# Performance work log

Measured on AMD Instinct MI355X. Metric: run time of the kernel, lower is better.

Reference implementation:

```python
import jax, jax.numpy as jnp
import numpy as np

K = 9          # knn_num
EPS = 1e-5     # BatchNorm eps


def _conv2d(x, w, stride):
    # x: NCHW, w: OIHW, VALID padding
    return jax.lax.conv_general_dilated(
        x, w, window_strides=stride, padding='VALID',
        dimension_numbers=('NCHW', 'OIHW', 'NCHW'))


def _bn_relu(x, gamma, beta):
    # training-mode BatchNorm2d (biased batch stats over N,H,W) + ReLU
    mean = jnp.mean(x, axis=(0, 2, 3), keepdims=True)
    var = jnp.var(x, axis=(0, 2, 3), keepdims=True)
    xhat = (x - mean) * jax.lax.rsqrt(var + EPS)
    return jax.nn.relu(xhat * gamma[None, :, None, None] + beta[None, :, None, None])


def setup_inputs() -> dict:
    key = jax.random.key(0)
    ks = jax.random.split(key, 5)
    B, C, N = 16, 128, 2048
    features = jax.random.normal(ks[0], (B, C, N, 1), dtype=jnp.float32)
    fan1 = 2 * C * 1 * 3
    W1 = jax.random.normal(ks[1], (C, 2 * C, 1, 3), dtype=jnp.float32) / np.sqrt(fan1)
    b1 = jnp.zeros((C,), dtype=jnp.float32)
    g1 = jnp.ones((C,), dtype=jnp.float32)
    beta1 = jnp.zeros((C,), dtype=jnp.float32)
    fan2 = C * 1 * 3
    W2 = jax.random.normal(ks[2], (C, C, 1, 3), dtype=jnp.float32) / np.sqrt(fan2)
    b2 = jnp.zeros((C,), dtype=jnp.float32)
    g2 = jnp.ones((C,), dtype=jnp.float32)
    beta2 = jnp.zeros((C,), dtype=jnp.float32)
    return {"features": features, "W1": W1, "b1": b1, "g1": g1, "beta1": beta1,
            "W2": W2, "b2": b2, "g2": g2, "beta2": beta2}


def reference(features, W1, b1, g1, beta1, W2, b2, g2, beta2):
    B, C, N, _ = features.shape
    x = features.reshape(B, C, N)
    # pairwise_distance[b,i,j] = -||x_i||^2 + 2 x_i.x_j - ||x_j||^2 = -||x_i - x_j||^2
    xx = jnp.sum(x * x, axis=1)                      # (B, N)
    inner = jnp.einsum('bci,bcj->bij', x, x)          # (B, N, N)
    pd = 2.0 * inner - xx[:, :, None] - xx[:, None, :]
    _, idx = jax.lax.top_k(pd, K)                     # (B, N, K) nearest neighbors (incl. self)
    xT = jnp.transpose(x, (0, 2, 1))                  # (B, N, C)
    feature = xT[jnp.arange(B)[:, None, None], idx]   # (B, N, K, C) gathered neighbors
    xc = xT[:, :, None, :]                            # (B, N, 1, C)
    diff = xc - feature
    # torch: cat(x, (x - f) - |x - f|) along channel dim -> (B, N, K, 2C)
    edge = jnp.concatenate(
        [jnp.broadcast_to(xc, diff.shape), diff - jnp.abs(diff)], axis=3)
    edge = jnp.transpose(edge, (0, 3, 1, 2))          # (B, 2C, N, K)
    h = _conv2d(edge, W1, (1, 3)) + b1[None, :, None, None]   # (B, C, N, 3)
    h = _bn_relu(h, g1, beta1)
    h = _conv2d(h, W2, (1, 1)) + b2[None, :, None, None]       # (B, C, N, 1)
    h = _bn_relu(h, g2, beta2)
    return h
```

## Files before the change

### kernel.cpp

```cpp
#include <hip/hip_runtime.h>
#include <cstddef>

#define BATCH 16
#define CH    128
#define NPTS  2048
#define KNN   9

typedef const __attribute__((address_space(1))) void* gptr_t;
typedef __attribute__((address_space(3))) void* lptr_t;

__global__ void k_transpose(const float* __restrict__ x, float* __restrict__ xT) {
  __shared__ float tile[32][33];
  int b = blockIdx.z;
  int n0 = blockIdx.x * 32, c0 = blockIdx.y * 32;
  int tx = threadIdx.x, ty = threadIdx.y;
#pragma unroll
  for (int i = 0; i < 4; ++i) {
    int cc = c0 + ty + i * 8;
    tile[ty + i * 8][tx] = x[((size_t)b * CH + cc) * NPTS + n0 + tx];
  }
  __syncthreads();
#pragma unroll
  for (int i = 0; i < 4; ++i) {
    int nn = n0 + ty + i * 8;
    xT[((size_t)b * NPTS + nn) * CH + c0 + tx] = tile[tx][ty + i * 8];
  }
}

__global__ void k_xx_pw(const float* __restrict__ x, float* __restrict__ xx) {
  int g = blockIdx.x * 256 + threadIdx.x;
  int b = g >> 11, n = g & (NPTS - 1);
  const float* p = x + (size_t)b * CH * NPTS + n;
  float s[128];
#pragma unroll
  for (int c = 0; c < 128; ++c) {
    float v = p[(size_t)c * NPTS];
    s[c] = __fmul_rn(v, v);
  }
  float lane[16];
#pragma unroll
  for (int l = 0; l < 16; ++l) {
    lane[l] = __fadd_rn(
        __fadd_rn(__fadd_rn(s[l], s[16 + l]), __fadd_rn(s[32 + l], s[48 + l])),
        __fadd_rn(__fadd_rn(s[64 + l], s[80 + l]), __fadd_rn(s[96 + l], s[112 + l])));
  }
  float m8[8];
#pragma unroll
  for (int i = 0; i < 8; ++i) m8[i] = __fadd_rn(lane[i], lane[i + 8]);
  float n4[4];
#pragma unroll
  for (int i = 0; i < 4; ++i) n4[i] = __fadd_rn(m8[i], m8[i + 4]);
  float p2[2];
#pragma unroll
  for (int i = 0; i < 2; ++i) p2[i] = __fadd_rn(n4[i], n4[i + 2]);
  xx[g] = __fadd_rn(p2[0], p2[1]);
}

__global__ __launch_bounds__(256) void k_knn_np(const float* __restrict__ x,
                                                const float* __restrict__ xx,
                                                int* __restrict__ idxout) {
  __shared__ __align__(16) char smraw[65536];
  float (*rowT)[64] = (float (*)[64])smraw;
  float (*colT)[64] = (float (*)[64])(smraw + 32768);
  float (*mv)[145] = (float (*)[145])smraw;
  unsigned short (*mi)[145] = (unsigned short (*)[145])(smraw + 37120);

  int b = blockIdx.y;
  int n0 = blockIdx.x * 64;
  int tid = threadIdx.x;
  int tx = tid & 15, ty = tid >> 4;

  const float* gb = x + (size_t)b * CH * NPTS;

#pragma unroll
  for (int i = 0; i < 8; ++i) {
    int e = i * 1024 + tid * 4;
    const float* ga = gb + (size_t)(e >> 6) * NPTS + n0 + (e & 63);
    __builtin_amdgcn_global_load_lds((gptr_t)ga, (lptr_t)(&rowT[0][0] + e), 16, 0, 0);
  }

  float tv[4][9];
  int   ti[4][9];
#pragma unroll
  for (int m = 0; m < 4; ++m)
#pragma unroll
    for (int s = 0; s < 9; ++s) { tv[m][s] = -3.4e38f; ti[m][s] = 0x7fffffff; }

  float xr[4];
#pragma unroll
  for (int m = 0; m < 4; ++m) xr[m] = xx[(size_t)b * NPTS + n0 + ty * 4 + m];

  for (int jt = 0; jt < NPTS; jt += 64) {
    __syncthreads();
#pragma unroll
    for (int i = 0; i < 8; ++i) {
      int e = i * 1024 + tid * 4;
      const float* ga = gb + (size_t)(e >> 6) * NPTS + jt + (e & 63);
      __builtin_amdgcn_global_load_lds((gptr_t)ga, (lptr_t)(&colT[0][0] + e), 16, 0, 0);
    }
    asm volatile("s_waitcnt vmcnt(0)" ::: "memory");
    __syncthreads();

    float acc[4][4];
#pragma unroll
    for (int m = 0; m < 4; ++m)
#pragma unroll
      for (int nn = 0; nn < 4; ++nn) acc[m][nn] = 0.f;

#pragma unroll 4
    for (int k = 0; k < CH; ++k) {
      float a[4], bv[4];
      *(float4*)a  = *(const float4*)&rowT[k][ty * 4];
      *(float4*)bv = *(const float4*)&colT[k][tx * 4];
#pragma unroll
      for (int m = 0; m < 4; ++m)
#pragma unroll
        for (int nn = 0; nn < 4; ++nn)
          acc[m][nn] = __builtin_fmaf(a[m], bv[nn], acc[m][nn]);
    }

#pragma unroll
    for (int nn = 0; nn < 4; ++nn) {
      int j = jt + tx * 4 + nn;
      float xc = xx[(size_t)b * NPTS + j];
#pragma unroll
      for (int m = 0; m < 4; ++m) {
        float val = __fsub_rn(__fsub_rn(__fmul_rn(2.0f, acc[m][nn]), xr[m]), xc);
        if (val > tv[m][8]) {
          float cv = val; int ci = j;
#pragma unroll
          for (int s = 0; s < 9; ++s) {
            bool sw = cv > tv[m][s];
            float t1 = tv[m][s]; int t2 = ti[m][s];
            tv[m][s] = sw ? cv : t1;  ti[m][s] = sw ? ci : t2;
            cv = sw ? t1 : cv;        ci = sw ? t2 : ci;
          }
        }
      }
    }
  }

  __syncthreads();
#pragma unroll
  for (int m = 0; m < 4; ++m) {
    int row = ty * 4 + m;
#pragma unroll
    for (int s = 0; s < 9; ++s) {
      mv[row][tx * 9 + s] = tv[m][s];
      mi[row][tx * 9 + s] = (unsigned short)ti[m][s];
    }
  }
  __syncthreads();
  if (tid < 64) {
    int row = tid;
    size_t base = ((size_t)b * NPTS + n0 + row) * KNN;
    for (int s = 0; s < KNN; ++s) {
      float best = -3.4e38f; int bj = 0x7fffffff; int bq = 0;
      for (int q = 0; q < 144; ++q) {
        float v = mv[row][q]; int jj = (int)mi[row][q];
        if (v > best || (v == best && jj < bj)) { best = v; bj = jj; bq = q; }
      }
      mv[row][bq] = -3.4e38f;
      idxout[base + s] = bj;
    }
  }
}

__global__ void k_prep(const float* __restrict__ W1, const float* __restrict__ W2,
                       float* __restrict__ At, float* __restrict__ W2t) {
  int g = blockIdx.x * 256 + threadIdx.x;
  if (g < 512 * 128) {
    int k = g / 128, o = g % 128;
    float v;
    if (k < 384) v = W1[(size_t)o * 768 + 384 + k];
    else {
      int c = k - 384;
      v = W1[(size_t)o * 768 + c * 3] + W1[(size_t)o * 768 + c * 3 + 1] +
          W1[(size_t)o * 768 + c * 3 + 2];
    }
    At[(size_t)k * 128 + o] = v;
  }
  if (g < 384 * 128) {
    int k = g / 128, o = g % 128;
    W2t[(size_t)k * 128 + o] = W2[(size_t)o * 384 + k];
  }
}

#define NN1 8
__global__ __launch_bounds__(256) void k_conv1(const float* __restrict__ xT,
                                               const int* __restrict__ knn_idx,
                                               const float* __restrict__ At,
                                               const float* __restrict__ bias1,
                                               float* __restrict__ h1) {
  __shared__ float dminL[NN1][KNN][132];
  __shared__ float xnL[NN1][132];
  __shared__ float AL[32][128];
  __shared__ int   idxL[NN1][KNN];
  int b = blockIdx.y;
  int n0 = blockIdx.x * NN1;
  int tid = threadIdx.x;

  if (tid < NN1 * KNN) {
    int n = tid / KNN, k = tid % KNN;
    idxL[n][k] = knn_idx[((size_t)b * NPTS + n0 + n) * KNN + k];
  }
  {
    int n = tid >> 5, q = tid & 31;
    float4 v = *(const float4*)&xT[((size_t)b * NPTS + n0 + n) * CH + q * 4];
    *(float4*)&xnL[n][q * 4] = v;
  }
  __syncthreads();
#pragma unroll
  for (int i = 0; i < 9; ++i) {
    int e = tid + i * 256;
    int rrow = e >> 5, q = e & 31;
    int n = rrow / KNN, k = rrow % KNN;
    int j = idxL[n][k];
    float4 xj = *(const float4*)&xT[((size_t)b * NPTS + j) * CH + q * 4];
    float4 xn = *(const float4*)&xnL[n][q * 4];
    float4 d;
    d.x = 2.0f * fminf(xn.x - xj.x, 0.0f);
    d.y = 2.0f * fminf(xn.y - xj.y, 0.0f);
    d.z = 2.0f * fminf(xn.z - xj.z, 0.0f);
    d.w = 2.0f * fminf(xn.w - xj.w, 0.0f);
    *(float4*)&dminL[n][k][q * 4] = d;
  }

  int n = tid & (NN1 - 1);
  int og = tid >> 3;
  float acc[4][3];
#pragma unroll
  for (int o = 0; o < 4; ++o)
#pragma unroll
    for (int t = 0; t < 3; ++t) acc[o][t] = 0.f;

  for (int kc = 0; kc < 16; ++kc) {
    __syncthreads();
#pragma unroll
    for (int i = 0; i < 4; ++i) {
      int e = tid + i * 256;
      int kk = e >> 5, q = e & 31;
      *(float4*)&AL[kk][q * 4] = *(const float4*)&At[(size_t)(kc * 32 + kk) * 128 + q * 4];
    }
    __syncthreads();
    if (kc < 12) {
#pragma unroll 4
      for (int kk = 0; kk < 32; ++kk) {
        int k = kc * 32 + kk;
        int c = k / 3, r = k - c * 3;
        float a[4];
        *(float4*)a = *(const float4*)&AL[kk][og * 4];
        float b0 = dminL[n][r][c];
        float b1 = dminL[n][3 + r][c];
        float b2 = dminL[n][6 + r][c];
#pragma unroll
        for (int o = 0; o < 4; ++o) {
          acc[o][0] = fmaf(a[o], b0, acc[o][0]);
          acc[o][1] = fmaf(a[o], b1, acc[o][1]);
          acc[o][2] = fmaf(a[o], b2, acc[o][2]);
        }
      }
    } else {
#pragma unroll 4
      for (int kk = 0; kk < 32; ++kk) {
        int c = (kc - 12) * 32 + kk;
        float a[4];
        *(float4*)a = *(const float4*)&AL[kk][og * 4];
        float b0 = xnL[n][c];
#pragma unroll
        for (int o = 0; o < 4; ++o) {
          acc[o][0] = fmaf(a[o], b0, acc[o][0]);
          acc[o][1] = fmaf(a[o], b0, acc[o][1]);
          acc[o][2] = fmaf(a[o], b0, acc[o][2]);
        }
      }
    }
  }
#pragma unroll
  for (int o = 0; o < 4; ++o) {
    int oo = og * 4 + o;
    float bs = bias1[oo];
    size_t base = ((size_t)(b * CH + oo) * NPTS + n0 + n) * 3;
#pragma unroll
    for (int t = 0; t < 3; ++t) h1[base + t] = acc[o][t] + bs;
  }
}

__global__ void k_stats_partial(const float* __restrict__ src, double* __restrict__ psum,
                                double* __restrict__ psq, int slablen) {
  __shared__ double ls[256], lq[256];
  int blk = blockIdx.x;
  const float* p = src + (size_t)blk * slablen;
  double s = 0.0, q = 0.0;
  for (int i = threadIdx.x; i < slablen; i += 256) {
    double v = (double)p[i];
    s += v; q = fma(v, v, q);
  }
  ls[threadIdx.x] = s; lq[threadIdx.x] = q;
  __syncthreads();
  for (int off = 128; off > 0; off >>= 1) {
    if (threadIdx.x < off) {
      ls[threadIdx.x] += ls[threadIdx.x + off];
      lq[threadIdx.x] += lq[threadIdx.x + off];
    }
    __syncthreads();
  }
  if (threadIdx.x == 0) { psum[blk] = ls[0]; psq[blk] = lq[0]; }
}

__global__ void k_stats_final(const double* __restrict__ psum, const double* __restrict__ psq,
                              const float* __restrict__ gamma, const float* __restrict__ beta,
                              float* __restrict__ aout, float* __restrict__ cout_,
                              double inv_n) {
  int c = threadIdx.x;
  if (c < CH) {
    double s = 0.0, q = 0.0;
    for (int b = 0; b < BATCH; ++b) { s += psum[b * CH + c]; q += psq[b * CH + c]; }
    double mean = s * inv_n;
    double var = q * inv_n - mean * mean;
    double a = (double)gamma[c] / sqrt(var + 1e-5);
    aout[c] = (float)a;
    cout_[c] = (float)((double)beta[c] - mean * a);
  }
}

__global__ __launch_bounds__(256) void k_conv2(const float* __restrict__ h1,
                                               const float* __restrict__ W2t,
                                               const float* __restrict__ bias2,
                                               const float* __restrict__ a1,
                                               const float* __restrict__ c1,
                                               float* __restrict__ out) {
  __shared__ float actL[384][36];
  __shared__ float WL[16][128];
  int b = blockIdx.y, n0 = blockIdx.x * 32, tid = threadIdx.x;
#pragma unroll
  for (int i = 0; i < 12; ++i) {
    int e = tid + i * 256;
    int c = e / 24, q = e % 24;
    float4 v = *(const float4*)&h1[((size_t)(b * CH + c) * NPTS + n0) * 3 + q * 4];
    float aa = a1[c], cc = c1[c];
    float vv[4] = {v.x, v.y, v.z, v.w};
#pragma unroll
    for (int s = 0; s < 4; ++s) {
      int f = q * 4 + s;
      int nn = f / 3, t = f - nn * 3;
      actL[c * 3 + t][nn] = fmaxf(0.0f, fmaf(vv[s], aa, cc));
    }
  }
  int ng = tid & 7, og = tid >> 3;
  float acc[4][4];
#pragma unroll
  for (int o = 0; o < 4; ++o)
#pragma unroll
    for (int nn = 0; nn < 4; ++nn) acc[o][nn] = 0.f;

  for (int kc = 0; kc < 24; ++kc) {
    __syncthreads();
#pragma unroll
    for (int i = 0; i < 2; ++i) {
      int e = tid + i * 256;
      int kk = e >> 5, q = e & 31;
      *(float4*)&WL[kk][q * 4] = *(const float4*)&W2t[(size_t)(kc * 16 + kk) * 128 + q * 4];
    }
    __syncthreads();
#pragma unroll 4
    for (int kk = 0; kk < 16; ++kk) {
      float a[4], bv[4];
      *(float4*)a  = *(const float4*)&WL[kk][og * 4];
      *(float4*)bv = *(const float4*)&actL[kc * 16 + kk][ng * 4];
#pragma unroll
      for (int o = 0; o < 4; ++o)
#pragma unroll
        for (int nn = 0; nn < 4; ++nn) acc[o][nn] = fmaf(a[o], bv[nn], acc[o][nn]);
    }
  }
#pragma unroll
  for (int o = 0; o < 4; ++o) {
    int oo = og * 4 + o;
    float bs = bias2[oo];
    size_t base = (size_t)(b * CH + oo) * NPTS + n0 + ng * 4;
#pragma unroll
    for (int nn = 0; nn < 4; ++nn) out[base + nn] = acc[o][nn] + bs;
  }
}

__global__ void k_bnrelu(float* __restrict__ out, const float* __restrict__ a2,
                         const float* __restrict__ c2) {
  int g = blockIdx.x * 256 + threadIdx.x;
  int c = (g >> 11) & 127;
  float v = out[g];
  out[g] = fmaxf(0.0f, fmaf(v, a2[c], c2[c]));
}

extern "C" void kernel_launch(void* const* d_in, const int* in_sizes, int n_in,
                              void* d_out, int out_size, void* d_ws, size_t ws_size,
                              hipStream_t stream) {
  const float* x   = (const float*)d_in[0];
  const float* W1  = (const float*)d_in[1];
  const float* b1  = (const float*)d_in[2];
  const float* g1  = (const float*)d_in[3];
  const float* be1 = (const float*)d_in[4];
  const float* W2  = (const float*)d_in[5];
  const float* b2  = (const float*)d_in[6];
  const float* g2  = (const float*)d_in[7];
  const float* be2 = (const float*)d_in[8];
  float* out = (float*)d_out;

  char* ws = (char*)d_ws;
  float*  xT      = (float*) (ws);
  float*  xx      = (float*) (ws + 16777216);
  int*    knn_idx = (int*)   (ws + 16908288);
  float*  At      = (float*) (ws + 18087936);
  float*  W2t     = (float*) (ws + 18350080);
  float*  h1      = (float*) (ws + 18546688);
  double* psum    = (double*)(ws + 68878336);
  double* psq     = (double*)(ws + 68894720);
  float*  a1      = (float*) (ws + 68911104);
  float*  c1      = (float*) (ws + 68911616);
  float*  a2      = (float*) (ws + 68912128);
  float*  c2      = (float*) (ws + 68912640);

  k_transpose<<<dim3(NPTS / 32, CH / 32, BATCH), dim3(32, 8), 0, stream>>>(x, xT);
  k_xx_pw<<<(BATCH * NPTS) / 256, 256, 0, stream>>>(x, xx);
  k_knn_np<<<dim3(NPTS / 64, BATCH), 256, 0, stream>>>(x, xx, knn_idx);
  k_prep<<<256, 256, 0, stream>>>(W1, W2, At, W2t);
  k_conv1<<<dim3(NPTS / NN1, BATCH), 256, 0, stream>>>(xT, knn_idx, At, b1, h1);
  k_stats_partial<<<BATCH * CH, 256, 0, stream>>>(h1, psum, psq, NPTS * 3);
  k_stats_final<<<1, 128, 0, stream>>>(psum, psq, g1, be1, a1, c1,
                                       1.0 / (double)(BATCH * NPTS * 3));
  k_conv2<<<dim3(NPTS / 32, BATCH), 256, 0, stream>>>(h1, W2t, b2, a1, c1, out);
  k_stats_partial<<<BATCH * CH, 256, 0, stream>>>(out, psum, psq, NPTS);
  k_stats_final<<<1, 128, 0, stream>>>(psum, psq, g2, be2, a2, c2,
                                       1.0 / (double)(BATCH * NPTS));
  k_bnrelu<<<(BATCH * CH * NPTS) / 256, 256, 0, stream>>>(out, a2, c2);
}
```

Measured before the change: 864.9 us.

## Enlarge kNN distance tile to 128x128 with 8x8 register blocking per thread

The kNN kernel's block tile grows from 64x64 to 128x128 points, and each thread now computes an 8x8 block of the inner-product matrix instead of 4x4. Dynamic LDS is raised to 128KB to hold the larger row and column panels. This raises arithmetic intensity per LDS read and halves the number of column-tile passes per block. In exchange it uses many more registers (a top-9 list for 8 rows plus 64 accumulators), and with one block per CU at 256 threads the grid drops to 256 blocks, so occupancy and latency hiding fall.

```diff
diff --git a/kernel.cpp b/kernel.cpp
--- a/kernel.cpp
+++ b/kernel.cpp
@@ -5,6 +5,8 @@
 #define CH    128
 #define NPTS  2048
 #define KNN   9
+#define BM    128
+#define BN    128
 
 typedef const __attribute__((address_space(1))) void* gptr_t;
 typedef __attribute__((address_space(3))) void* lptr_t;
@@ -56,102 +58,107 @@
   xx[g] = __fadd_rn(p2[0], p2[1]);
 }
 
-__global__ __launch_bounds__(256) void k_knn_np(const float* __restrict__ x,
-                                                const float* __restrict__ xx,
-                                                int* __restrict__ idxout) {
-  __shared__ __align__(16) char smraw[65536];
-  float (*rowT)[64] = (float (*)[64])smraw;
-  float (*colT)[64] = (float (*)[64])(smraw + 32768);
-  float (*mv)[145] = (float (*)[145])smraw;
-  unsigned short (*mi)[145] = (unsigned short (*)[145])(smraw + 37120);
+__global__ __launch_bounds__(256, 1) void k_knn_np(const float* __restrict__ x,
+                                                   const float* __restrict__ xx,
+                                                   int* __restrict__ idxout) {
+  extern __shared__ __align__(16) char smraw[];
+  float (*rowT)[BM] = (float (*)[BM])smraw;
+  float (*colT)[BN] = (float (*)[BN])(smraw + 65536);
+  float (*mv)[144] = (float (*)[144])smraw;
+  unsigned short (*mi)[144] = (unsigned short (*)[144])(smraw + 73728);
 
   int b = blockIdx.y;
-  int n0 = blockIdx.x * 64;
+  int n0 = blockIdx.x * BM;
   int tid = threadIdx.x;
   int tx = tid & 15, ty = tid >> 4;
 
   const float* gb = x + (size_t)b * CH * NPTS;
 
 #pragma unroll
-  for (int i = 0; i < 8; ++i) {
+  for (int i = 0; i < 16; ++i) {
     int e = i * 1024 + tid * 4;
-    const float* ga = gb + (size_t)(e >> 6) * NPTS + n0 + (e & 63);
+    const float* ga = gb + (size_t)(e >> 7) * NPTS + n0 + (e & 127);
     __builtin_amdgcn_global_load_lds((gptr_t)ga, (lptr_t)(&rowT[0][0] + e), 16, 0, 0);
   }
 
-  float tv[4][9];
-  int   ti[4][9];
-#pragma unroll
-  for (int m = 0; m < 4; ++m)
-#pragma unroll
-    for (int s = 0; s < 9; ++s) { tv[m][s] = -3.4e38f; ti[m][s] = 0x7fffffff; }
-
-  float xr[4];
-#pragma unroll
-  for (int m = 0; m < 4; ++m) xr[m] = xx[(size_t)b * NPTS + n0 + ty * 4 + m];
-
-  for (int jt = 0; jt < NPTS; jt += 64) {
-    __syncthreads();
-#pragma unroll
-    for (int i = 0; i < 8; ++i) {
+  float tv[8][9];
+  int   ti[8][9];
+#pragma unroll
+  for (int r = 0; r < 8; ++r)
+#pragma unroll
+    for (int s = 0; s < 9; ++s) { tv[r][s] = -3.4e38f; ti[r][s] = 0x7fffffff; }
+
+  float xr[8];
+#pragma unroll
+  for (int r = 0; r < 8; ++r)
+    xr[r] = xx[(size_t)b * NPTS + n0 + (r >> 2) * 64 + ty * 4 + (r & 3)];
+
+  for (int jt = 0; jt < NPTS; jt += BN) {
+    __syncthreads();
+#pragma unroll
+    for (int i = 0; i < 16; ++i) {
       int e = i * 1024 + tid * 4;
-      const float* ga = gb + (size_t)(e >> 6) * NPTS + jt + (e & 63);
+      const float* ga = gb + (size_t)(e >> 7) * NPTS + jt + (e & 127);
       __builtin_amdgcn_global_load_lds((gptr_t)ga, (lptr_t)(&colT[0][0] + e), 16, 0, 0);
     }
     asm volatile("s_waitcnt vmcnt(0)" ::: "memory");
     __syncthreads();
 
-    float acc[4][4];
-#pragma unroll
-    for (int m = 0; m < 4; ++m)
-#pragma unroll
-      for (int nn = 0; nn < 4; ++nn) acc[m][nn] = 0.f;
+    float acc[8][8];
+#pragma unroll
+    for (int r = 0; r < 8; ++r)
+#pragma unroll
+      for (int c = 0; c < 8; ++c) acc[r][c] = 0.f;
 
 #pragma unroll 4
     for (int k = 0; k < CH; ++k) {
-      float a[4], bv[4];
-      *(float4*)a  = *(const float4*)&rowT[k][ty * 4];
-      *(float4*)bv = *(const float4*)&colT[k][tx * 4];
-#pragma unroll
-      for (int m = 0; m < 4; ++m)
-#pragma unroll
-        for (int nn = 0; nn < 4; ++nn)
-          acc[m][nn] = __builtin_fmaf(a[m], bv[nn], acc[m][nn]);
-    }
-
-#pragma unroll
-    for (int nn = 0; nn < 4; ++nn) {
-      int j = jt + tx * 4 + nn;
-      float xc = xx[(size_t)b * NPTS + j];
-#pragma unroll
-      for (int m = 0; m < 4; ++m) {
-        float val = __fsub_rn(__fsub_rn(__fmul_rn(2.0f, acc[m][nn]), xr[m]), xc);
-        if (val > tv[m][8]) {
-          float cv = val; int ci = j;
-#pragma unroll
-          for (int s = 0; s < 9; ++s) {
-            bool sw = cv > tv[m][s];
-            float t1 = tv[m][s]; int t2 = ti[m][s];
-            tv[m][s] = sw ? cv : t1;  ti[m][s] = sw ? ci : t2;
-            cv = sw ? t1 : cv;        ci = sw ? t2 : ci;
+      float a[8], bv[8];
+      *(float4*)&a[0]  = *(const float4*)&rowT[k][ty * 4];
+      *(float4*)&a[4]  = *(const float4*)&rowT[k][64 + ty * 4];
+      *(float4*)&bv[0] = *(const float4*)&colT[k][tx * 4];
+      *(float4*)&bv[4] = *(const float4*)&colT[k][64 + tx * 4];
+#pragma unroll
+      for (int r = 0; r < 8; ++r)
+#pragma unroll
+        for (int c = 0; c < 8; ++c)
+          acc[r][c] = __builtin_fmaf(a[r], bv[c], acc[r][c]);
+    }
+
+#pragma unroll
+    for (int g = 0; g < 2; ++g)
+#pragma unroll
+      for (int nn = 0; nn < 4; ++nn) {
+        int j = jt + g * 64 + tx * 4 + nn;
+        float xc = xx[(size_t)b * NPTS + j];
+#pragma unroll
+        for (int r = 0; r < 8; ++r) {
+          float val = __fsub_rn(__fsub_rn(__fmul_rn(2.0f, acc[r][g * 4 + nn]), xr[r]), xc);
+          if (val > tv[r][8]) {
+            float cv = val; int ci = j;
+#pragma unroll
+            for (int s = 0; s < 9; ++s) {
+              bool sw = cv > tv[r][s];
+              float t1 = tv[r][s]; int t2 = ti[r][s];
+              tv[r][s] = sw ? cv : t1;  ti[r][s] = sw ? ci : t2;
+              cv = sw ? t1 : cv;        ci = sw ? t2 : ci;
+            }
           }
         }
       }
-    }
   }
 
   __syncthreads();
 #pragma unroll
-  for (int m = 0; m < 4; ++m) {
-    int row = ty * 4 + m;
+  for (int r = 0; r < 8; ++r) {
+    int row = (r >> 2) * 64 + ty * 4 + (r & 3);
 #pragma unroll
     for (int s = 0; s < 9; ++s) {
-      mv[row][tx * 9 + s] = tv[m][s];
-      mi[row][tx * 9 + s] = (unsigned short)ti[m][s];
+      mv[row][tx * 9 + s] = tv[r][s];
+      mi[row][tx * 9 + s] = (unsigned short)ti[r][s];
     }
   }
   __syncthreads();
-  if (tid < 64) {
+  if (tid < 128) {
     int row = tid;
     size_t base = ((size_t)b * NPTS + n0 + row) * KNN;
     for (int s = 0; s < KNN; ++s) {
@@ -420,9 +427,16 @@
   float*  a2      = (float*) (ws + 68912128);
   float*  c2      = (float*) (ws + 68912640);
 
+  static int lds_attr_set = 0;
+  if (!lds_attr_set) {
+    (void)hipFuncSetAttribute((const void*)k_knn_np,
+                              hipFuncAttributeMaxDynamicSharedMemorySize, 131072);
+    lds_attr_set = 1;
+  }
+
   k_transpose<<<dim3(NPTS / 32, CH / 32, BATCH), dim3(32, 8), 0, stream>>>(x, xT);
   k_xx_pw<<<(BATCH * NPTS) / 256, 256, 0, stream>>>(x, xx);
-  k_knn_np<<<dim3(NPTS / 64, BATCH), 256, 0, stream>>>(x, xx, knn_idx);
+  k_knn_np<<<dim3(NPTS / BM, BATCH), 256, 131072, stream>>>(x, xx, knn_idx);
   k_prep<<<256, 256, 0, stream>>>(W1, W2, At, W2t);
   k_conv1<<<dim3(NPTS / NN1, BATCH), 256, 0, stream>>>(xT, knn_idx, At, b1, h1);
   k_stats_partial<<<BATCH * CH, 256, 0, stream>>>(h1, psum, psq, NPTS * 3);
```

Result: slower. 1.172 ms (+35.5%).

## Split KNN column tile into two channel halves and overlap loads with compute

Applied to the files above, without the earlier changes.

The column tile in the KNN distance kernel is split into two 64-channel halves held in separate LDS buffers. Each half is loaded asynchronously while the other half's FMA loop runs, using partial vmcnt waits and raw s_barrier instead of a full drain. This is meant to hide global-to-LDS latency behind the inner-product compute. The wrap-around prefetch on the last tile does redundant work, and correctness depends on the vmcnt counts matching the outstanding loads. The first-half loop also depends on the earlier rowT loads having completed under the vmcnt(4) wait.

```diff
diff --git a/kernel.cpp b/kernel.cpp
--- a/kernel.cpp
+++ b/kernel.cpp
@@ -61,7 +61,8 @@
                                                 int* __restrict__ idxout) {
   __shared__ __align__(16) char smraw[65536];
   float (*rowT)[64] = (float (*)[64])smraw;
-  float (*colT)[64] = (float (*)[64])(smraw + 32768);
+  float* colA = (float*)(smraw + 32768);
+  float* colB = (float*)(smraw + 49152);
   float (*mv)[145] = (float (*)[145])smraw;
   unsigned short (*mi)[145] = (unsigned short (*)[145])(smraw + 37120);
 
@@ -90,16 +91,25 @@
 #pragma unroll
   for (int m = 0; m < 4; ++m) xr[m] = xx[(size_t)b * NPTS + n0 + ty * 4 + m];
 
+#pragma unroll
+  for (int i = 0; i < 4; ++i) {
+    int e = i * 1024 + tid * 4;
+    const float* ga = gb + (size_t)(e >> 6) * NPTS + 0 + (e & 63);
+    __builtin_amdgcn_global_load_lds((gptr_t)ga, (lptr_t)(colA + e), 16, 0, 0);
+  }
+
   for (int jt = 0; jt < NPTS; jt += 64) {
-    __syncthreads();
-#pragma unroll
-    for (int i = 0; i < 8; ++i) {
+    int jnext = (jt + 64) & (NPTS - 1);
+
+    __builtin_amdgcn_s_barrier();
+#pragma unroll
+    for (int i = 0; i < 4; ++i) {
       int e = i * 1024 + tid * 4;
-      const float* ga = gb + (size_t)(e >> 6) * NPTS + jt + (e & 63);
-      __builtin_amdgcn_global_load_lds((gptr_t)ga, (lptr_t)(&colT[0][0] + e), 16, 0, 0);
-    }
-    asm volatile("s_waitcnt vmcnt(0)" ::: "memory");
-    __syncthreads();
+      const float* ga = gb + (size_t)(64 + (e >> 6)) * NPTS + jt + (e & 63);
+      __builtin_amdgcn_global_load_lds((gptr_t)ga, (lptr_t)(colB + e), 16, 0, 0);
+    }
+    asm volatile("s_waitcnt vmcnt(4)" ::: "memory");
+    __builtin_amdgcn_s_barrier();
 
     float acc[4][4];
 #pragma unroll
@@ -107,11 +117,33 @@
 #pragma unroll
       for (int nn = 0; nn < 4; ++nn) acc[m][nn] = 0.f;
 
-#pragma unroll 4
-    for (int k = 0; k < CH; ++k) {
+#pragma unroll 8
+    for (int k2 = 0; k2 < 64; ++k2) {
       float a[4], bv[4];
-      *(float4*)a  = *(const float4*)&rowT[k][ty * 4];
-      *(float4*)bv = *(const float4*)&colT[k][tx * 4];
+      *(float4*)a  = *(const float4*)&rowT[k2][ty * 4];
+      *(float4*)bv = *(const float4*)(colA + k2 * 64 + tx * 4);
+#pragma unroll
+      for (int m = 0; m < 4; ++m)
+#pragma unroll
+        for (int nn = 0; nn < 4; ++nn)
+          acc[m][nn] = __builtin_fmaf(a[m], bv[nn], acc[m][nn]);
+    }
+
+    __builtin_amdgcn_s_barrier();
+#pragma unroll
+    for (int i = 0; i < 4; ++i) {
+      int e = i * 1024 + tid * 4;
+      const float* ga = gb + (size_t)(e >> 6) * NPTS + jnext + (e & 63);
+      __builtin_amdgcn_global_load_lds((gptr_t)ga, (lptr_t)(colA + e), 16, 0, 0);
+    }
+    asm volatile("s_waitcnt vmcnt(4)" ::: "memory");
+    __builtin_amdgcn_s_barrier();
+
+#pragma unroll 8
+    for (int k2 = 0; k2 < 64; ++k2) {
+      float a[4], bv[4];
+      *(float4*)a  = *(const float4*)&rowT[64 + k2][ty * 4];
+      *(float4*)bv = *(const float4*)(colB + k2 * 64 + tx * 4);
 #pragma unroll
       for (int m = 0; m < 4; ++m)
 #pragma unroll
```

Result: no change. 863.5 us (-0.2%).
